# Kernel tuning notes

Measured on AMD Instinct MI355X. Metric: run time of the kernel, lower is better.

## Reference

```python
import jax, jax.numpy as jnp
import numpy as np

B, L, DIM = 1, 2048, 512
DHEAD = 64
HEADS = DIM // DHEAD  # 8
KS = 127              # kernel_size (odd)
EXP = 4


def setup_inputs() -> dict:
    key = jax.random.key(0)
    ks = jax.random.split(key, 8)
    sc = 0.02
    rnd = lambda k, shape: (jax.random.normal(k, shape, jnp.float32) * sc)
    return {
        "x": jax.random.normal(ks[0], (B, L, DIM), jnp.float32),
        "ln1_g": jnp.ones((DIM,), jnp.float32),
        "ln1_b": jnp.zeros((DIM,), jnp.float32),
        "qkv_w": rnd(ks[1], (DIM, 3 * DIM)),
        "qkv_b": jnp.zeros((3 * DIM,), jnp.float32),
        "rpb": rnd(ks[2], (HEADS, 2 * KS - 1)),
        "proj_w": rnd(ks[3], (DIM, DIM)),
        "proj_b": jnp.zeros((DIM,), jnp.float32),
        "ln2_g": jnp.ones((DIM,), jnp.float32),
        "ln2_b": jnp.zeros((DIM,), jnp.float32),
        "ff1_w": rnd(ks[4], (DIM, DIM * EXP)),
        "ff1_b": jnp.zeros((DIM * EXP,), jnp.float32),
        "ff2_w": rnd(ks[5], (DIM * EXP, DIM)),
        "ff2_b": jnp.zeros((DIM,), jnp.float32),
    }


def _layernorm(x, g, b, eps=1e-5):
    m = x.mean(-1, keepdims=True)
    v = ((x - m) ** 2).mean(-1, keepdims=True)
    return (x - m) * jax.lax.rsqrt(v + eps) * g + b


def _neighborhood_attn_1d(x, qkv_w, qkv_b, rpb, proj_w, proj_b):
    # NATTEN NeighborhoodAttention1D: window of KS keys per query, clamped
    # at sequence edges so every query sees exactly KS keys (requires L >= KS).
    b, l, dim = x.shape
    qkv = (x @ qkv_w + qkv_b).reshape(b, l, 3, HEADS, DHEAD)
    q, k, v = qkv[:, :, 0], qkv[:, :, 1], qkv[:, :, 2]  # [b,l,h,d]
    scale = DHEAD ** -0.5
    # window start per query, clamped to stay in-bounds
    starts = jnp.clip(jnp.arange(l) - KS // 2, 0, l - KS)          # [l]
    idx = starts[:, None] + jnp.arange(KS)                         # [l,KS]
    kg = k[:, idx]                                                 # [b,l,KS,h,d]
    vg = v[:, idx]                                                 # [b,l,KS,h,d]
    logits = jnp.einsum('blhd,blkhd->blhk', q * scale, kg)         # [b,l,h,KS]
    # relative-position bias: index = (j - i) + (KS - 1), in [0, 2KS-2]
    bias_idx = idx - jnp.arange(l)[:, None] + (KS - 1)             # [l,KS]
    logits = logits + rpb[:, bias_idx].transpose(1, 0, 2)[None]    # [1,l,h,KS]
    attn = jax.nn.softmax(logits, axis=-1)
    out = jnp.einsum('blhk,blkhd->blhd', attn, vg).reshape(b, l, dim)
    return out @ proj_w + proj_b


def reference(x, ln1_g, ln1_b, qkv_w, qkv_b, rpb, proj_w, proj_b,
              ln2_g, ln2_b, ff1_w, ff1_b, ff2_w, ff2_b):
    x = x + _neighborhood_attn_1d(_layernorm(x, ln1_g, ln1_b),
                                  qkv_w, qkv_b, rpb, proj_w, proj_b)
    h = _layernorm(x, ln2_g, ln2_b)
    h = jax.nn.gelu(h @ ff1_w + ff1_b, approximate=False) @ ff2_w + ff2_b
    return x + h
```

## Files before the change

### kernel.cpp

```cpp
#include <hip/hip_runtime.h>
#include <hip/hip_bf16.h>

static constexpr int Lc     = 2048;
static constexpr int DIMc   = 512;
static constexpr int HEADSc = 8;
static constexpr int DHEADc = 64;
static constexpr int KSc    = 127;
static constexpr int NQKVc  = 1536;

typedef __attribute__((ext_vector_type(8))) short short8;
typedef __attribute__((ext_vector_type(4))) float f32x4;
typedef unsigned short u16;
typedef unsigned int u32;

__device__ __forceinline__ float b2f(u16 s) {
  return __uint_as_float(((u32)s) << 16);
}
__device__ __forceinline__ u16 f2b(float x) {
  u32 u = __float_as_uint(x);
  return (u16)((u + 0x7fffu + ((u >> 16) & 1u)) >> 16);
}
__device__ __forceinline__ void gload16(const void* g, void* l) {
  __builtin_amdgcn_global_load_lds(
      (const __attribute__((address_space(1))) u32*)g,
      (__attribute__((address_space(3))) u32*)l, 16, 0, 0);
}

__global__ __launch_bounds__(256) void prep_kernel(
    const float* __restrict__ w0, const float* __restrict__ w1,
    const float* __restrict__ w2, const float* __restrict__ w3,
    u16* __restrict__ o0, u16* __restrict__ o1, u16* __restrict__ o2,
    u16* __restrict__ o3, const float* __restrict__ xin,
    const float* __restrict__ g, const float* __restrict__ b,
    u16* __restrict__ lnout) {
  __shared__ float tl[32][33];
  __shared__ float rs[4], rq[4], stat[2];
  const int tid = threadIdx.x;
  if (blockIdx.x >= 3072) {
    const int row = blockIdx.x - 3072;
    const float* rp = xin + (size_t)row * DIMc;
    float v0 = rp[tid];
    float v1 = rp[tid + 256];
    float s = v0 + v1;
    float sq = v0 * v0 + v1 * v1;
#pragma unroll
    for (int o = 32; o > 0; o >>= 1) {
      s += __shfl_down(s, o);
      sq += __shfl_down(sq, o);
    }
    const int wid = tid >> 6, lane = tid & 63;
    if (lane == 0) { rs[wid] = s; rq[wid] = sq; }
    __syncthreads();
    if (tid == 0) {
      float S = rs[0] + rs[1] + rs[2] + rs[3];
      float Q = rq[0] + rq[1] + rq[2] + rq[3];
      float m = S / DIMc;
      float var = Q / DIMc - m * m;
      stat[0] = m;
      stat[1] = rsqrtf(var + 1e-5f);
    }
    __syncthreads();
    const float m = stat[0], r = stat[1];
    lnout[(size_t)row * DIMc + tid] = f2b((v0 - m) * r * g[tid] + b[tid]);
    lnout[(size_t)row * DIMc + tid + 256] =
        f2b((v1 - m) * r * g[tid + 256] + b[tid + 256]);
    return;
  }
  int t = blockIdx.x;
  const float* W;
  u16* O;
  int K, N;
  if (t < 768)       { W = w0; O = o0; K = 512;  N = 1536; }
  else if (t < 1024) { W = w1; O = o1; K = 512;  N = 512;  t -= 768; }
  else if (t < 2048) { W = w2; O = o2; K = 512;  N = 2048; t -= 1024; }
  else               { W = w3; O = o3; K = 2048; N = 512;  t -= 2048; }
  const int nt = N >> 5;
  const int by = t / nt, bx = t % nt;
  const int c = tid & 31, r0 = tid >> 5;
#pragma unroll
  for (int i = 0; i < 4; ++i) {
    const int r = r0 + i * 8;
    tl[r][c] = W[(size_t)(by * 32 + r) * N + bx * 32 + c];
  }
  __syncthreads();
#pragma unroll
  for (int i = 0; i < 4; ++i) {
    const int r = r0 + i * 8;
    O[(size_t)(bx * 32 + r) * K + by * 32 + c] = f2b(tl[c][r]);
  }
}

__global__ __launch_bounds__(256) void ln2x_kernel(
    const u16* __restrict__ parts, const float* __restrict__ x,
    const float* __restrict__ pb, const float* __restrict__ g,
    const float* __restrict__ b, float* __restrict__ x2,
    u16* __restrict__ lnout) {
  const int row = blockIdx.x;
  const int tid = threadIdx.x;
  const size_t base = (size_t)row * DIMc;
  float v0, v1;
  {
    const int c0 = tid, c1 = tid + 256;
    v0 = x[base + c0] + pb[c0] + b2f(parts[base + c0]) +
         b2f(parts[(size_t)Lc * DIMc + base + c0]);
    v1 = x[base + c1] + pb[c1] + b2f(parts[base + c1]) +
         b2f(parts[(size_t)Lc * DIMc + base + c1]);
  }
  x2[base + tid] = v0;
  x2[base + tid + 256] = v1;
  float s = v0 + v1;
  float sq = v0 * v0 + v1 * v1;
  __shared__ float rs[4], rq[4], stat[2];
#pragma unroll
  for (int o = 32; o > 0; o >>= 1) {
    s += __shfl_down(s, o);
    sq += __shfl_down(sq, o);
  }
  const int wid = tid >> 6, lane = tid & 63;
  if (lane == 0) { rs[wid] = s; rq[wid] = sq; }
  __syncthreads();
  if (tid == 0) {
    float S = rs[0] + rs[1] + rs[2] + rs[3];
    float Q = rq[0] + rq[1] + rq[2] + rq[3];
    float m = S / DIMc;
    float var = Q / DIMc - m * m;
    stat[0] = m;
    stat[1] = rsqrtf(var + 1e-5f);
  }
  __syncthreads();
  const float m = stat[0], r = stat[1];
  lnout[base + tid] = f2b((v0 - m) * r * g[tid] + b[tid]);
  lnout[base + tid + 256] = f2b((v1 - m) * r * g[tid + 256] + b[tid + 256]);
}

template <int OP, int SPLIT, typename OUT_T>
__global__ __launch_bounds__(128) void mfma_gemm(
    const u16* __restrict__ A, const u16* __restrict__ Bt,
    const float* __restrict__ bias, OUT_T* __restrict__ C, int M, int N,
    int K) {
  constexpr int BK = 64;
  __shared__ __align__(16) u16 As[2][64 * BK];
  __shared__ __align__(16) u16 Bs[2][64 * BK];
  const int tid = threadIdx.x;
  const int wave = tid >> 6, lane = tid & 63;
  const int m0 = blockIdx.y * 64, n0 = blockIdx.x * 64;
  const int wn = wave * 32;
  const int z = (SPLIT > 1) ? blockIdx.z : 0;
  const int kslice = K / SPLIT;
  const int kbeg = z * kslice;
  const int T = kslice / BK;

  f32x4 acc[4][2] = {};

  const int fr = lane & 15;
  const int hi = lane >> 4;

  const int lrow = wave * 8 + (lane >> 3);
  const int lcol = ((lane & 7) ^ (lane >> 3)) * 8;

#define STAGE(k0, buf)                                                        \
  {                                                                           \
    _Pragma("unroll") for (int p = 0; p < 4; ++p) {                           \
      gload16(A + (size_t)(m0 + p * 16 + lrow) * K + (k0) + lcol,             \
              &As[buf][p * 1024 + wave * 512]);                               \
      gload16(Bt + (size_t)(n0 + p * 16 + lrow) * K + (k0) + lcol,            \
              &Bs[buf][p * 1024 + wave * 512]);                               \
    }                                                                         \
  }

  STAGE(kbeg, 0);
  __syncthreads();

  for (int t = 0; t < T; ++t) {
    const int cur = t & 1;
    if (t + 1 < T) STAGE(kbeg + (t + 1) * BK, cur ^ 1);

    short8 af[4][2], bf[2][2];
#pragma unroll
    for (int i = 0; i < 4; ++i) {
      const int row = i * 16 + fr;
      const char* rb = (const char*)As[cur] + row * 128;
#pragma unroll
      for (int ks = 0; ks < 2; ++ks)
        af[i][ks] =
            *(const short8*)(rb + ((ks * 64 + hi * 16) ^ ((fr & 7) << 4)));
    }
#pragma unroll
    for (int j = 0; j < 2; ++j) {
      const int row = wn + j * 16 + fr;
      const char* rb = (const char*)Bs[cur] + row * 128;
#pragma unroll
      for (int ks = 0; ks < 2; ++ks)
        bf[j][ks] =
            *(const short8*)(rb + ((ks * 64 + hi * 16) ^ ((fr & 7) << 4)));
    }
#pragma unroll
    for (int ks = 0; ks < 2; ++ks)
#pragma unroll
      for (int i = 0; i < 4; ++i)
#pragma unroll
        for (int j = 0; j < 2; ++j)
          acc[i][j] = __builtin_amdgcn_mfma_f32_16x16x32_bf16(
              af[i][ks], bf[j][ks], acc[i][j], 0, 0, 0);
    __syncthreads();
  }
#undef STAGE

  const int cl = lane & 15;
  const int rbase = (lane >> 4) * 4;
#pragma unroll
  for (int i = 0; i < 4; ++i) {
#pragma unroll
    for (int j = 0; j < 2; ++j) {
      const int c = n0 + wn + j * 16 + cl;
      const float bv = (OP == 3) ? 0.f : bias[c];
#pragma unroll
      for (int r = 0; r < 4; ++r) {
        const int row = m0 + i * 16 + rbase + r;
        float v = acc[i][j][r] + bv;
        if (OP == 1) v = 0.5f * v * (1.0f + erff(v * 0.70710678118f));
        const size_t o = (size_t)row * N + c;
        if (OP == 3) {
          ((u16*)C)[(size_t)z * M * N + o] = f2b(v);
        } else {
          ((u16*)C)[o] = f2b(v);
        }
      }
    }
  }
}

__global__ __launch_bounds__(256) void ff2_reduce(const u16* __restrict__ part,
                                                  const float* __restrict__ x2,
                                                  const float* __restrict__ bias,
                                                  float* __restrict__ out) {
  const int i = blockIdx.x * 256 + threadIdx.x;
  const size_t b = (size_t)i * 4;
  const int col = (int)(b & (DIMc - 1));
  const float4 r = *(const float4*)(x2 + b);
  const float4 bb = *(const float4*)(bias + col);
  float4 s = {r.x + bb.x, r.y + bb.y, r.z + bb.z, r.w + bb.w};
#pragma unroll
  for (int zz = 0; zz < 4; ++zz) {
    const ushort4 p =
        *(const ushort4*)(part + (size_t)zz * (Lc * DIMc) + b);
    s.x += b2f(p.x);
    s.y += b2f(p.y);
    s.z += b2f(p.z);
    s.w += b2f(p.w);
  }
  *(float4*)(out + b) = s;
}

__global__ __launch_bounds__(256) void attn_mfma(const u16* __restrict__ qkv,
                                                 const float* __restrict__ rpb,
                                                 u16* __restrict__ out) {
  constexpr int NR = 192, NT = 12, PP = 200;
  __shared__ __align__(16) u16 Ks[NR * DHEADc];
  __shared__ __align__(16) u16 Vt[DHEADc * NR];
  __shared__ __align__(16) u16 Ps[4][16 * PP];
  __shared__ float rp[2 * KSc - 1];
  const int h = blockIdx.y, l0 = blockIdx.x * 64, tid = threadIdx.x;
  const int wv = tid >> 6, lane = tid & 63;
  const int fr = lane & 15, hi = lane >> 4;

  int s_min = l0 - 63;
  if (s_min < 0) s_min = 0;
  if (s_min > Lc - KSc) s_min = Lc - KSc;

  for (int i = tid; i < 2 * KSc - 1; i += 256) rp[i] = rpb[h * (2 * KSc - 1) + i];

#pragma unroll
  for (int rd = 0; rd < 6; ++rd) {
    const int linear = rd * 4096 + wv * 1024 + lane * 16;
    const int row = linear >> 7;
    const int seg = (linear >> 4) & 7;
    const int segp = seg ^ (row & 7);
    int gl = s_min + row;
    if (gl > Lc - 1) gl = Lc - 1;
    gload16(qkv + (size_t)gl * NQKVc + DIMc + h * DHEADc + segp * 8,
            (char*)Ks + rd * 4096 + wv * 1024);
  }

#pragma unroll
  for (int rd = 0; rd < 3; ++rd) {
    const int t = rd * 256 + tid;
    const int rpair = t >> 3, seg = t & 7;
    const int r0 = rpair * 2;
    int g0 = s_min + r0, g1 = s_min + r0 + 1;
    if (g0 > Lc - 1) g0 = Lc - 1;
    if (g1 > Lc - 1) g1 = Lc - 1;
    const short8 a =
        *(const short8*)(qkv + (size_t)g0 * NQKVc + 2 * DIMc + h * DHEADc + seg * 8);
    const short8 bq =
        *(const short8*)(qkv + (size_t)g1 * NQKVc + 2 * DIMc + h * DHEADc + seg * 8);
#pragma unroll
    for (int j = 0; j < 8; ++j) {
      const int d = seg * 8 + j;
      int byte = d * (NR * 2) + r0 * 2;
      byte ^= (d & 7) << 4;
      *(u32*)((char*)Vt + byte) =
          ((u32)(u16)a[j]) | (((u32)(u16)bq[j]) << 16);
    }
  }

  const int lq = l0 + wv * 16 + fr;
  short8 qf[2];
#pragma unroll
  for (int ks = 0; ks < 2; ++ks)
    qf[ks] = *(const short8*)(qkv + (size_t)lq * NQKVc + h * DHEADc + ks * 32 + hi * 8);

  __syncthreads();

  f32x4 S[NT] = {};
#pragma unroll
  for (int jt = 0; jt < NT; ++jt) {
#pragma unroll
    for (int ks = 0; ks < 2; ++ks) {
      int byte = (jt * 16 + fr) * 128 + ks * 64 + hi * 16;
      byte ^= (fr & 7) << 4;
      const short8 kf = *(const short8*)((const char*)Ks + byte);
      S[jt] = __builtin_amdgcn_mfma_f32_16x16x32_bf16(qf[ks], kf, S[jt], 0, 0, 0);
    }
  }

  float inv4[4];
#pragma unroll
  for (int r = 0; r < 4; ++r) {
    const int l = l0 + wv * 16 + hi * 4 + r;
    int st = l - 63;
    if (st < 0) st = 0;
    if (st > Lc - KSc) st = Lc - KSc;
    float mx = -3e38f;
#pragma unroll
    for (int jt = 0; jt < NT; ++jt) {
      const int pos = s_min + jt * 16 + fr;
      const int j = pos - st;
      float v = -3e38f;
      if (j >= 0 && j <= KSc - 1) v = S[jt][r] * 0.125f + rp[pos - l + KSc - 1];
      S[jt][r] = v;
      mx = fmaxf(mx, v);
    }
#pragma unroll
    for (int o = 1; o < 16; o <<= 1) mx = fmaxf(mx, __shfl_xor(mx, o));
    float sum = 0.f;
#pragma unroll
    for (int jt = 0; jt < NT; ++jt) {
      const float e = __expf(S[jt][r] - mx);
      S[jt][r] = e;
      sum += e;
    }
#pragma unroll
    for (int o = 1; o < 16; o <<= 1) sum += __shfl_xor(sum, o);
    inv4[r] = 1.f / sum;
  }

#pragma unroll
  for (int jt = 0; jt < NT; ++jt)
#pragma unroll
    for (int r = 0; r < 4; ++r)
      Ps[wv][(hi * 4 + r) * PP + jt * 16 + fr] = f2b(S[jt][r] * inv4[r]);

  f32x4 O[4] = {};
#pragma unroll
  for (int ks = 0; ks < 6; ++ks) {
    const short8 pa =
        *(const short8*)((const char*)Ps[wv] + fr * (PP * 2) + ks * 64 + hi * 16);
#pragma unroll
    for (int dt = 0; dt < 4; ++dt) {
      int byte = (dt * 16 + fr) * (NR * 2) + ks * 64 + hi * 16;
      byte ^= (fr & 7) << 4;
      const short8 vb = *(const short8*)((const char*)Vt + byte);
      O[dt] = __builtin_amdgcn_mfma_f32_16x16x32_bf16(pa, vb, O[dt], 0, 0, 0);
    }
  }

#pragma unroll
  for (int dt = 0; dt < 4; ++dt)
#pragma unroll
    for (int r = 0; r < 4; ++r)
      out[(size_t)(l0 + wv * 16 + hi * 4 + r) * DIMc + h * DHEADc + dt * 16 + fr] =
          f2b(O[dt][r]);
}

extern "C" void kernel_launch(void* const* d_in, const int* in_sizes, int n_in,
                              void* d_out, int out_size, void* d_ws,
                              size_t ws_size, hipStream_t stream) {
  const float* x      = (const float*)d_in[0];
  const float* ln1_g  = (const float*)d_in[1];
  const float* ln1_b  = (const float*)d_in[2];
  const float* qkv_w  = (const float*)d_in[3];
  const float* qkv_b  = (const float*)d_in[4];
  const float* rpb    = (const float*)d_in[5];
  const float* proj_w = (const float*)d_in[6];
  const float* proj_b = (const float*)d_in[7];
  const float* ln2_g  = (const float*)d_in[8];
  const float* ln2_b  = (const float*)d_in[9];
  const float* ff1_w  = (const float*)d_in[10];
  const float* ff1_b  = (const float*)d_in[11];
  const float* ff2_w  = (const float*)d_in[12];
  const float* ff2_b  = (const float*)d_in[13];
  float* out = (float*)d_out;

  char* ws = (char*)d_ws;
  u16*   lnbuf   = (u16*)(ws);
  u16*   qkvbuf  = (u16*)(ws + ((size_t)2  << 20));
  u16*   attnbuf = (u16*)(ws + ((size_t)8  << 20));
  float* x2      = (float*)(ws + ((size_t)10 << 20));
  u16*   ff1buf  = (u16*)(ws + ((size_t)14 << 20));
  u16*   wt_qkv  = (u16*)(ws + ((size_t)22 << 20));
  u16*   wt_proj = (u16*)(ws + ((size_t)23 << 20) + ((size_t)512 << 10));
  u16*   wt_ff1  = (u16*)(ws + ((size_t)24 << 20));
  u16*   wt_ff2  = (u16*)(ws + ((size_t)26 << 20));
  u16*   parts   = (u16*)(ws + ((size_t)2  << 20));

  prep_kernel<<<5120, 256, 0, stream>>>(qkv_w, proj_w, ff1_w, ff2_w, wt_qkv,
                                        wt_proj, wt_ff1, wt_ff2, x, ln1_g,
                                        ln1_b, lnbuf);
  mfma_gemm<0, 1, u16><<<dim3(NQKVc / 64, Lc / 64), 128, 0, stream>>>(
      lnbuf, wt_qkv, qkv_b, qkvbuf, Lc, NQKVc, DIMc);
  attn_mfma<<<dim3(Lc / 64, HEADSc), 256, 0, stream>>>(qkvbuf, rpb, attnbuf);
  mfma_gemm<3, 2, u16><<<dim3(DIMc / 64, Lc / 64, 2), 128, 0, stream>>>(
      attnbuf, wt_proj, nullptr, parts, Lc, DIMc, DIMc);
  ln2x_kernel<<<Lc, 256, 0, stream>>>(parts, x, proj_b, ln2_g, ln2_b, x2, lnbuf);
  mfma_gemm<1, 1, u16><<<dim3(4 * DIMc / 64, Lc / 64), 128, 0, stream>>>(
      lnbuf, wt_ff1, ff1_b, ff1buf, Lc, 4 * DIMc, DIMc);
  mfma_gemm<3, 4, u16><<<dim3(DIMc / 64, Lc / 64, 4), 128, 0, stream>>>(
      ff1buf, wt_ff2, nullptr, parts, Lc, DIMc, 4 * DIMc);
  ff2_reduce<<<(Lc * DIMc / 4) / 256, 256, 0, stream>>>(parts, x2, ff2_b, out);
}
```

Baseline: 73.79 us.

## Drop split-K for proj/ff2 GEMMs, fuse residual epilogue, deepen GEMM prefetch

```diff
diff --git a/kernel.cpp b/kernel.cpp
--- a/kernel.cpp
+++ b/kernel.cpp
@@ -90,24 +90,15 @@
   }
 }
 
-__global__ __launch_bounds__(256) void ln2x_kernel(
-    const u16* __restrict__ parts, const float* __restrict__ x,
-    const float* __restrict__ pb, const float* __restrict__ g,
-    const float* __restrict__ b, float* __restrict__ x2,
-    u16* __restrict__ lnout) {
+__global__ __launch_bounds__(256) void ln2_kernel(const float* __restrict__ in,
+                                                  const float* __restrict__ g,
+                                                  const float* __restrict__ b,
+                                                  u16* __restrict__ out) {
   const int row = blockIdx.x;
   const int tid = threadIdx.x;
-  const size_t base = (size_t)row * DIMc;
-  float v0, v1;
-  {
-    const int c0 = tid, c1 = tid + 256;
-    v0 = x[base + c0] + pb[c0] + b2f(parts[base + c0]) +
-         b2f(parts[(size_t)Lc * DIMc + base + c0]);
-    v1 = x[base + c1] + pb[c1] + b2f(parts[base + c1]) +
-         b2f(parts[(size_t)Lc * DIMc + base + c1]);
-  }
-  x2[base + tid] = v0;
-  x2[base + tid + 256] = v1;
+  const float* rp = in + (size_t)row * DIMc;
+  float v0 = rp[tid];
+  float v1 = rp[tid + 256];
   float s = v0 + v1;
   float sq = v0 * v0 + v1 * v1;
   __shared__ float rs[4], rq[4], stat[2];
@@ -129,15 +120,16 @@
   }
   __syncthreads();
   const float m = stat[0], r = stat[1];
-  lnout[base + tid] = f2b((v0 - m) * r * g[tid] + b[tid]);
-  lnout[base + tid + 256] = f2b((v1 - m) * r * g[tid + 256] + b[tid + 256]);
-}
-
-template <int OP, int SPLIT, typename OUT_T>
+  out[(size_t)row * DIMc + tid] = f2b((v0 - m) * r * g[tid] + b[tid]);
+  out[(size_t)row * DIMc + tid + 256] =
+      f2b((v1 - m) * r * g[tid + 256] + b[tid + 256]);
+}
+
+template <int OP, typename OUT_T>
 __global__ __launch_bounds__(128) void mfma_gemm(
     const u16* __restrict__ A, const u16* __restrict__ Bt,
-    const float* __restrict__ bias, OUT_T* __restrict__ C, int M, int N,
-    int K) {
+    const float* __restrict__ bias, const float* __restrict__ res,
+    OUT_T* __restrict__ C, int M, int N, int K) {
   constexpr int BK = 64;
   __shared__ __align__(16) u16 As[2][64 * BK];
   __shared__ __align__(16) u16 Bs[2][64 * BK];
@@ -145,10 +137,7 @@
   const int wave = tid >> 6, lane = tid & 63;
   const int m0 = blockIdx.y * 64, n0 = blockIdx.x * 64;
   const int wn = wave * 32;
-  const int z = (SPLIT > 1) ? blockIdx.z : 0;
-  const int kslice = K / SPLIT;
-  const int kbeg = z * kslice;
-  const int T = kslice / BK;
+  const int T = K / BK;
 
   f32x4 acc[4][2] = {};
 
@@ -168,12 +157,17 @@
     }                                                                         \
   }
 
-  STAGE(kbeg, 0);
-  __syncthreads();
+  STAGE(0, 0);
+  STAGE(BK, 1);
 
   for (int t = 0; t < T; ++t) {
     const int cur = t & 1;
-    if (t + 1 < T) STAGE(kbeg + (t + 1) * BK, cur ^ 1);
+    if (t + 1 < T) {
+      asm volatile("s_waitcnt vmcnt(8)" ::: "memory");
+    } else {
+      asm volatile("s_waitcnt vmcnt(0)" ::: "memory");
+    }
+    __builtin_amdgcn_s_barrier();
 
     short8 af[4][2], bf[2][2];
 #pragma unroll
@@ -194,6 +188,12 @@
         bf[j][ks] =
             *(const short8*)(rb + ((ks * 64 + hi * 16) ^ ((fr & 7) << 4)));
     }
+    asm volatile("s_waitcnt lgkmcnt(0)" ::: "memory");
+    __builtin_amdgcn_sched_barrier(0);
+    __builtin_amdgcn_s_barrier();
+
+    if (t + 2 < T) STAGE((t + 2) * BK, cur);
+
 #pragma unroll
     for (int ks = 0; ks < 2; ++ks)
 #pragma unroll
@@ -202,7 +202,6 @@
         for (int j = 0; j < 2; ++j)
           acc[i][j] = __builtin_amdgcn_mfma_f32_16x16x32_bf16(
               af[i][ks], bf[j][ks], acc[i][j], 0, 0, 0);
-    __syncthreads();
   }
 #undef STAGE
 
@@ -213,43 +212,21 @@
 #pragma unroll
     for (int j = 0; j < 2; ++j) {
       const int c = n0 + wn + j * 16 + cl;
-      const float bv = (OP == 3) ? 0.f : bias[c];
+      const float bv = bias[c];
 #pragma unroll
       for (int r = 0; r < 4; ++r) {
         const int row = m0 + i * 16 + rbase + r;
         float v = acc[i][j][r] + bv;
         if (OP == 1) v = 0.5f * v * (1.0f + erff(v * 0.70710678118f));
         const size_t o = (size_t)row * N + c;
-        if (OP == 3) {
-          ((u16*)C)[(size_t)z * M * N + o] = f2b(v);
+        if (OP == 2) {
+          ((float*)C)[o] = v + res[o];
         } else {
           ((u16*)C)[o] = f2b(v);
         }
       }
     }
   }
-}
-
-__global__ __launch_bounds__(256) void ff2_reduce(const u16* __restrict__ part,
-                                                  const float* __restrict__ x2,
-                                                  const float* __restrict__ bias,
-                                                  float* __restrict__ out) {
-  const int i = blockIdx.x * 256 + threadIdx.x;
-  const size_t b = (size_t)i * 4;
-  const int col = (int)(b & (DIMc - 1));
-  const float4 r = *(const float4*)(x2 + b);
-  const float4 bb = *(const float4*)(bias + col);
-  float4 s = {r.x + bb.x, r.y + bb.y, r.z + bb.z, r.w + bb.w};
-#pragma unroll
-  for (int zz = 0; zz < 4; ++zz) {
-    const ushort4 p =
-        *(const ushort4*)(part + (size_t)zz * (Lc * DIMc) + b);
-    s.x += b2f(p.x);
-    s.y += b2f(p.y);
-    s.z += b2f(p.z);
-    s.w += b2f(p.w);
-  }
-  *(float4*)(out + b) = s;
 }
 
 __global__ __launch_bounds__(256) void attn_mfma(const u16* __restrict__ qkv,
@@ -412,20 +389,18 @@
   u16*   wt_proj = (u16*)(ws + ((size_t)23 << 20) + ((size_t)512 << 10));
   u16*   wt_ff1  = (u16*)(ws + ((size_t)24 << 20));
   u16*   wt_ff2  = (u16*)(ws + ((size_t)26 << 20));
-  u16*   parts   = (u16*)(ws + ((size_t)2  << 20));
 
   prep_kernel<<<5120, 256, 0, stream>>>(qkv_w, proj_w, ff1_w, ff2_w, wt_qkv,
                                         wt_proj, wt_ff1, wt_ff2, x, ln1_g,
                                         ln1_b, lnbuf);
-  mfma_gemm<0, 1, u16><<<dim3(NQKVc / 64, Lc / 64), 128, 0, stream>>>(
-      lnbuf, wt_qkv, qkv_b, qkvbuf, Lc, NQKVc, DIMc);
+  mfma_gemm<0, u16><<<dim3(NQKVc / 64, Lc / 64), 128, 0, stream>>>(
+      lnbuf, wt_qkv, qkv_b, nullptr, qkvbuf, Lc, NQKVc, DIMc);
   attn_mfma<<<dim3(Lc / 64, HEADSc), 256, 0, stream>>>(qkvbuf, rpb, attnbuf);
-  mfma_gemm<3, 2, u16><<<dim3(DIMc / 64, Lc / 64, 2), 128, 0, stream>>>(
-      attnbuf, wt_proj, nullptr, parts, Lc, DIMc, DIMc);
-  ln2x_kernel<<<Lc, 256, 0, stream>>>(parts, x, proj_b, ln2_g, ln2_b, x2, lnbuf);
-  mfma_gemm<1, 1, u16><<<dim3(4 * DIMc / 64, Lc / 64), 128, 0, stream>>>(
-      lnbuf, wt_ff1, ff1_b, ff1buf, Lc, 4 * DIMc, DIMc);
-  mfma_gemm<3, 4, u16><<<dim3(DIMc / 64, Lc / 64, 4), 128, 0, stream>>>(
-      ff1buf, wt_ff2, nullptr, parts, Lc, DIMc, 4 * DIMc);
-  ff2_reduce<<<(Lc * DIMc / 4) / 256, 256, 0, stream>>>(parts, x2, ff2_b, out);
-}
+  mfma_gemm<2, float><<<dim3(DIMc / 64, Lc / 64), 128, 0, stream>>>(
+      attnbuf, wt_proj, proj_b, x, x2, Lc, DIMc, DIMc);
+  ln2_kernel<<<Lc, 256, 0, stream>>>(x2, ln2_g, ln2_b, lnbuf);
+  mfma_gemm<1, u16><<<dim3(4 * DIMc / 64, Lc / 64), 128, 0, stream>>>(
+      lnbuf, wt_ff1, ff1_b, nullptr, ff1buf, Lc, 4 * DIMc, DIMc);
+  mfma_gemm<2, float><<<dim3(DIMc / 64, Lc / 64), 128, 0, stream>>>(
+      ff1buf, wt_ff2, ff2_b, x2, out, Lc, DIMc, 4 * DIMc);
+}
```

Measured after the change: 72.84 us. About the same (-1.3%).
